# Kernel tuning notes

Hardware: AMD Instinct MI355X
Metric: run time of the kernel (lower is better)

## Reference

```python
import jax, jax.numpy as jnp
import numpy as np
import math

NUM_BUCKETS = 32
MAX_DISTANCE = 128
N_HEADS = 16
D_KV = 64
ATTN_SCALE = True


def _relative_position_bucket(relative_position, num_buckets=NUM_BUCKETS, max_distance=MAX_DISTANCE):
    # bidirectional (encoder) variant
    nb = num_buckets // 2
    buckets = (relative_position > 0).astype(jnp.int32) * nb
    rp = jnp.abs(relative_position)
    max_exact = nb // 2
    is_small = rp < max_exact
    rp_large = max_exact + (
        jnp.log(rp.astype(jnp.float32) / max_exact)
        / math.log(max_distance / max_exact)
        * (nb - max_exact)
    ).astype(jnp.int32)
    rp_large = jnp.minimum(rp_large, nb - 1)
    buckets = buckets + jnp.where(is_small, rp, rp_large)
    return buckets


def compute_bias(rel_bias_emb, q_len, k_len):
    ctx = jnp.arange(q_len)[:, None]
    mem = jnp.arange(k_len)[None, :]
    bucket = _relative_position_bucket(mem - ctx)  # [q,k] int32 in [0,32)
    values = rel_bias_emb[bucket]                  # [q,k,H]
    return jnp.transpose(values, (2, 0, 1))[None]  # [1,H,q,k]


def setup_inputs() -> dict:
    key = jax.random.key(0)
    k1, k2, k3, k4 = jax.random.split(key, 4)
    B, S, D = 2, 2048, 1024
    return {
        "hidden_states": jax.random.normal(k1, (B, S, D), jnp.float32),
        "attention_mask": jnp.ones((B, 1, S, S), jnp.float32),
        "W_qkv": jax.random.normal(k2, (D, 3 * D), jnp.float32) * 0.02,
        "W_o": jax.random.normal(k3, (D, D), jnp.float32) * 0.02,
        "rel_bias_emb": jax.random.normal(k4, (NUM_BUCKETS, N_HEADS), jnp.float32) * 0.02,
    }


def reference(hidden_states, attention_mask, W_qkv, W_o, rel_bias_emb):
    B, S, D = hidden_states.shape
    # fused QKV projection (no bias), then split as in split_tensor_along_last_dim
    qkv = jnp.einsum("bsd,de->bse", hidden_states, W_qkv)
    q, k, v = jnp.split(qkv, 3, axis=-1)
    # [b,s,H*d] -> [b,H,s,d]
    def to_heads(t):
        return jnp.transpose(t.reshape(B, S, N_HEADS, D_KV), (0, 2, 1, 3))
    q, k, v = to_heads(q), to_heads(k), to_heads(v)
    scores = jnp.einsum("bhqd,bhkd->bhqk", q, k)
    if ATTN_SCALE:
        scores = scores / math.sqrt(D_KV)
    position_bias = compute_bias(rel_bias_emb, S, S)  # [1,H,S,S]
    scores = scores * attention_mask + (-10000.0 * (1.0 - attention_mask) + position_bias)
    probs = jax.nn.softmax(scores, axis=-1)  # dropout = eval mode (identity)
    ctx = jnp.einsum("bhqk,bhkd->bhqd", probs, v)
    ctx = jnp.transpose(ctx, (0, 2, 1, 3)).reshape(B, S, N_HEADS * D_KV)
    attn_output = jnp.einsum("bse,ed->bsd", ctx, W_o)
    return attn_output
```

## Files before the change

kernel.cpp:

```cpp
#include <hip/hip_runtime.h>
#include <cstdint>

#define DEV static __device__ __forceinline__

typedef __bf16 bf16x8 __attribute__((ext_vector_type(8)));
typedef __bf16 bf16x4 __attribute__((ext_vector_type(4)));
typedef short  s16x4  __attribute__((ext_vector_type(4)));
typedef float  f32x4  __attribute__((ext_vector_type(4)));

DEV unsigned short f32_bf16(float f) {
  union { float f; unsigned u; } v; v.f = f;
  unsigned r = v.u + 0x7FFFu + ((v.u >> 16) & 1u);
  return (unsigned short)(r >> 16);
}

DEV void gload16(const void* g, void* lds) {
  __builtin_amdgcn_global_load_lds((__attribute__((address_space(1))) void*)g,
                                   (__attribute__((address_space(3))) void*)lds,
                                   16, 0, 0);
}

DEV float bcast_lane(float v, int srclane) {
  union { float f; int i; } u; u.f = v;
  u.i = __builtin_amdgcn_ds_bpermute(srclane << 2, u.i);
  return u.f;
}

DEV f32x4 mfma16_bf16(bf16x4 a, bf16x4 b, f32x4 c) {
  union { bf16x4 h; s16x4 s; } ua, ub; ua.h = a; ub.h = b;
#if __has_builtin(__builtin_amdgcn_mfma_f32_16x16x16bf16_1k)
  return __builtin_amdgcn_mfma_f32_16x16x16bf16_1k(ua.s, ub.s, c, 0, 0, 0);
#else
  f32x4 d;
  asm("v_mfma_f32_16x16x16_bf16 %0, %1, %2, %3" : "=v"(d) : "v"(ua.s), "v"(ub.s), "v"(c));
  return d;
#endif
}

__global__ void cast_bf16(const float* __restrict__ x, unsigned short* __restrict__ y) {
  int i = blockIdx.x * 256 + threadIdx.x;
  float4 v = ((const float4*)x)[i];
  uint2 o;
  o.x = (unsigned)f32_bf16(v.x) | ((unsigned)f32_bf16(v.y) << 16);
  o.y = (unsigned)f32_bf16(v.z) | ((unsigned)f32_bf16(v.w) << 16);
  ((uint2*)y)[i] = o;
}

__global__ void transpose_cast(const float* __restrict__ W, unsigned short* __restrict__ WT,
                               int K, int N) {
  __shared__ float t[64][65];
  int k0 = blockIdx.x * 64, n0 = blockIdx.y * 64;
  int tn = threadIdx.x & 63, tk = threadIdx.x >> 6;
#pragma unroll
  for (int i = 0; i < 64; i += 4)
    t[tk + i][tn] = W[(size_t)(k0 + tk + i) * N + n0 + tn];
  __syncthreads();
  int k2 = (threadIdx.x & 31) * 2, n = threadIdx.x >> 5;
#pragma unroll
  for (int i = 0; i < 64; i += 8) {
    int nn = n + i;
    unsigned o = (unsigned)f32_bf16(t[k2][nn]) | ((unsigned)f32_bf16(t[k2 + 1][nn]) << 16);
    *(unsigned*)&WT[(size_t)(n0 + nn) * K + k0 + k2] = o;
  }
}

__global__ void mask_check(const float* __restrict__ m, int* __restrict__ flag) {
  size_t i = ((size_t)blockIdx.x * 256 + threadIdx.x) * 4;
  float4 v = *(const float4*)(m + i);
  if (v.x != 1.0f || v.y != 1.0f || v.z != 1.0f || v.w != 1.0f) atomicOr(flag, 1);
}

template <int MODE, int TN>
__global__ void __launch_bounds__(256) gemm_bt(const unsigned short* __restrict__ A,
                                               const unsigned short* __restrict__ BT,
                                               float* __restrict__ Cout,
                                               unsigned short* __restrict__ Qb,
                                               unsigned short* __restrict__ Kb,
                                               unsigned short* __restrict__ VTb,
                                               int M, int N, int K) {
  constexpr int NT = TN / 32;
  __shared__ __align__(16) unsigned short As[128 * 32];
  __shared__ __align__(16) unsigned short Bs[TN * 32];
  const int tid = threadIdx.x, wave = tid >> 6, lane = tid & 63;
  const int l = lane & 15, quad = lane >> 4;
  const int wm = (wave & 1) * 64, wn = (wave >> 1) * (TN >> 1);
  const int bm = blockIdx.x, bn = blockIdx.y;

  const int srowA = wave * 32 + (lane >> 2);
  const int sswzA = ((lane & 3) ^ (srowA & 3)) * 8;
  const int srowB = (TN == 128) ? srowA : (wave * 16 + (lane >> 2));
  const int sswzB = ((lane & 3) ^ (srowB & 3)) * 8;
  const unsigned short* pA = A + (size_t)(bm * 128 + srowA) * K + sswzA;
  const unsigned short* pB = BT + (size_t)(bn * TN + srowB) * K + sswzB;
  unsigned short* ldsA0 = &As[(wave * 32) * 32];
  unsigned short* ldsA1 = &As[(wave * 32 + 16) * 32];
  unsigned short* ldsB0 = &Bs[((TN == 128 ? wave * 32 : wave * 16)) * 32];
  unsigned short* ldsB1 = &Bs[(wave * 32 + 16) * 32];

  f32x4 acc[4][NT];
#pragma unroll
  for (int i = 0; i < 4; i++)
#pragma unroll
    for (int j = 0; j < NT; j++) { f32x4 z = {0.f, 0.f, 0.f, 0.f}; acc[i][j] = z; }

  for (int kt = 0; kt < K; kt += 32) {
    __syncthreads();
    gload16(pA, ldsA0);
    gload16(pA + (size_t)16 * K, ldsA1);
    gload16(pB, ldsB0);
    if (TN == 128) gload16(pB + (size_t)16 * K, ldsB1);
    pA += 32; pB += 32;
    __syncthreads();
    bf16x8 af[4], bv[NT];
#pragma unroll
    for (int mt = 0; mt < 4; mt++) {
      int r = wm + mt * 16 + l;
      af[mt] = *(const bf16x8*)&As[r * 32 + ((quad ^ (r & 3)) * 8)];
    }
#pragma unroll
    for (int nt = 0; nt < NT; nt++) {
      int r = wn + nt * 16 + l;
      bv[nt] = *(const bf16x8*)&Bs[r * 32 + ((quad ^ (r & 3)) * 8)];
    }
#pragma unroll
    for (int mt = 0; mt < 4; mt++)
#pragma unroll
      for (int nt = 0; nt < NT; nt++)
        acc[mt][nt] = __builtin_amdgcn_mfma_f32_16x16x32_bf16(af[mt], bv[nt], acc[mt][nt], 0, 0, 0);
  }

#pragma unroll
  for (int nt = 0; nt < NT; nt++) {
    const int col = bn * TN + wn + nt * 16 + l;
#pragma unroll
    for (int mt = 0; mt < 4; mt++) {
      const int row0 = bm * 128 + wm + mt * 16 + quad * 4;
      if (MODE == 0) {
#pragma unroll
        for (int r = 0; r < 4; r++)
          Cout[(size_t)(row0 + r) * N + col] = acc[mt][nt][r];
      } else {
        const int bb = row0 >> 11, s = row0 & 2047;
        if (col < 2048) {
          unsigned short* dst = (col < 1024) ? Qb : Kb;
          const int c = col & 1023;
          const size_t off = ((size_t)(bb * 16 + (c >> 6)) * 2048 + s) * 64 + (c & 63);
#pragma unroll
          for (int r = 0; r < 4; r++)
            dst[off + (size_t)r * 64] = f32_bf16(acc[mt][nt][r]);
        } else {
          const int c = col - 2048;
          const int sl = s & 127;
          const int snew = (s & ~127) | (sl & 0x63) | ((sl & 0x0C) << 1) | ((sl & 0x10) >> 2);
          const size_t off = ((size_t)(bb * 16 + (c >> 6)) * 64 + (c & 63)) * 2048 + snew;
          bf16x4 pk;
#pragma unroll
          for (int r = 0; r < 4; r++) pk[r] = (__bf16)acc[mt][nt][r];
          *(bf16x4*)&VTb[off] = pk;
        }
      }
    }
  }
}

__global__ void __launch_bounds__(512, 4) attn(const unsigned short* __restrict__ Qb,
                                               const unsigned short* __restrict__ Kb,
                                               const unsigned short* __restrict__ VTb,
                                               const float* __restrict__ mask,
                                               const float* __restrict__ emb,
                                               const int* __restrict__ mflag,
                                               unsigned short* __restrict__ ctx) {
  __shared__ __align__(16) unsigned short KV[2][16384];
  __shared__ float biasLUT[512];

  const float LOG2E = 1.4426950408889634f;
  const float c1 = 0.125f * LOG2E;
  const float C2 = 10000.0f * LOG2E;
  const int tid = threadIdx.x, wave = tid >> 6, lane = tid & 63;
  const int l = lane & 15, quad = lane >> 4;
  const int wq = wave & 3, wk = wave >> 2;
  const int bh = blockIdx.x & 31, qt = blockIdx.x >> 5;
  const int b = bh >> 4, h = bh & 15;
  const int q0 = qt * 128;

  {
    int i = tid;
    int rel = i - 256;
    int rp = rel < 0 ? -rel : rel;
    int off = rp < 8 ? rp
                     : 8 + (rp >= 12) + (rp >= 16) + (rp >= 23) + (rp >= 32) +
                           (rp >= 46) + (rp >= 64) + (rp >= 91);
    int bucket = (rel > 0 ? 16 : 0) + off;
    biasLUT[i] = emb[bucket * 16 + h] * LOG2E;
  }
  const float satL = emb[15 * 16 + h] * LOG2E;
  const float satH = emb[31 * 16 + h] * LOG2E;
  const int masked = *mflag;

  const unsigned short* qb  = Qb  + ((size_t)(b * 16 + h) * 2048 + q0) * 64;
  const unsigned short* kb  = Kb  + (size_t)(b * 16 + h) * 2048 * 64;
  const unsigned short* vtb = VTb + (size_t)(b * 16 + h) * 64 * 2048;
  const float* mbase = mask + (size_t)b * 2048 * 2048;

  const int rw8 = lane >> 3, c8s = lane & 7;
  const int rw16 = lane >> 4, c16 = lane & 15;

#pragma unroll
  for (int j = 0; j < 2; j++) {
    int row = wave * 16 + j * 8 + rw8;
    gload16(qb + (size_t)row * 64 + ((c8s ^ (row & 7)) * 8), &KV[1][(wave * 16 + j * 8) * 64]);
  }
#pragma unroll
  for (int j = 0; j < 2; j++) {
    int row = wave * 16 + j * 8 + rw8;
    gload16(kb + (size_t)row * 64 + ((c8s ^ (row & 7)) * 8), &KV[0][(wave * 16 + j * 8) * 64]);
  }
#pragma unroll
  for (int j = 0; j < 2; j++) {
    int drow = wave * 8 + j * 4 + rw16;
    gload16(vtb + (size_t)drow * 2048 + ((c16 ^ (drow & 7)) * 8),
            &KV[0][8192 + (wave * 8 + j * 4) * 128]);
  }
  __syncthreads();

  bf16x8 qf[2][2];
#pragma unroll
  for (int mtq = 0; mtq < 2; mtq++)
#pragma unroll
    for (int ks = 0; ks < 2; ks++) {
      int row = wq * 32 + mtq * 16 + l;
      qf[mtq][ks] = *(const bf16x8*)&KV[1][row * 64 + (((ks * 4 + quad) ^ (row & 7)) * 8)];
    }
  __syncthreads();

#pragma unroll
  for (int j = 0; j < 2; j++) {
    int row = wave * 16 + j * 8 + rw8;
    gload16(kb + (size_t)(128 + row) * 64 + ((c8s ^ (row & 7)) * 8),
            &KV[1][(wave * 16 + j * 8) * 64]);
  }
#pragma unroll
  for (int j = 0; j < 2; j++) {
    int drow = wave * 8 + j * 4 + rw16;
    gload16(vtb + (size_t)drow * 2048 + 128 + ((c16 ^ (drow & 7)) * 8),
            &KV[1][8192 + (wave * 8 + j * 4) * 128]);
  }

  float lr[2] = {0.f, 0.f};
  f32x4 Oa[2][4];
#pragma unroll
  for (int mtq = 0; mtq < 2; mtq++)
#pragma unroll
    for (int dt = 0; dt < 4; dt++) { f32x4 z = {0.f, 0.f, 0.f, 0.f}; Oa[mtq][dt] = z; }

  for (int kt = 0; kt < 16; kt++) {
    const int k0 = kt * 128;
    const unsigned short* Ks  = KV[kt & 1];
    const unsigned short* VTs = KV[kt & 1] + 8192;

    const int d0 = k0 - q0;
    const bool sat = (d0 >= 256) || (d0 <= -256);
    const float bias_u = d0 > 0 ? satH : satL;
    const int ibase = 256 + d0 + wk * 64 + quad * 4 - wq * 32 - l;

#pragma unroll
    for (int p = 0; p < 2; p++) {
      bf16x4 pa[2][2];
#pragma unroll
      for (int t = 0; t < 2; t++) {
        const int ntk = p * 2 + t;
        int row = wk * 64 + ntk * 16 + l;
        bf16x8 kf0 = *(const bf16x8*)&Ks[row * 64 + ((quad ^ (row & 7)) * 8)];
        bf16x8 kf1 = *(const bf16x8*)&Ks[row * 64 + (((4 + quad) ^ (row & 7)) * 8)];
#pragma unroll
        for (int mtq = 0; mtq < 2; mtq++) {
          f32x4 s = {0.f, 0.f, 0.f, 0.f};
          s = __builtin_amdgcn_mfma_f32_16x16x32_bf16(kf0, qf[mtq][0], s, 0, 0, 0);
          s = __builtin_amdgcn_mfma_f32_16x16x32_bf16(kf1, qf[mtq][1], s, 0, 0, 0);

          const int ib = ibase + ntk * 16 - mtq * 16;
          if (!masked) {
            if (sat) {
#pragma unroll
              for (int r = 0; r < 4; r++) s[r] = fmaf(s[r], c1, bias_u);
            } else {
#pragma unroll
              for (int r = 0; r < 4; r++) s[r] = fmaf(s[r], c1, biasLUT[ib + r]);
            }
          } else {
            const int qg = q0 + wq * 32 + mtq * 16 + l;
            const int kg = k0 + wk * 64 + ntk * 16 + quad * 4;
            float4 mv4 = *(const float4*)&mbase[(size_t)qg * 2048 + kg];
#pragma unroll
            for (int r = 0; r < 4; r++) {
              float mv = r == 0 ? mv4.x : (r == 1 ? mv4.y : (r == 2 ? mv4.z : mv4.w));
              float bias = sat ? bias_u : biasLUT[ib + r];
              s[r] = fmaf(s[r], mv * c1, fmaf(mv, C2, bias - C2));
            }
          }
          bf16x4 pk;
          float ls = 0.f;
#pragma unroll
          for (int r = 0; r < 4; r++) {
            float pv = __builtin_amdgcn_exp2f(s[r]);
            ls += pv;
            pk[r] = (__bf16)pv;
          }
          lr[mtq] += ls;
          pa[mtq][t] = pk;
        }
      }

#pragma unroll
      for (int dt = 0; dt < 4; dt++) {
        int row = dt * 16 + l;
        bf16x8 w = *(const bf16x8*)&VTs[row * 128 + (((wk * 8 + p * 4 + quad) ^ (l & 7)) * 8)];
        bf16x4 vlo = __builtin_shufflevector(w, w, 0, 1, 2, 3);
        bf16x4 vhi = __builtin_shufflevector(w, w, 4, 5, 6, 7);
#pragma unroll
        for (int mtq = 0; mtq < 2; mtq++) {
          Oa[mtq][dt] = mfma16_bf16(pa[mtq][0], vlo, Oa[mtq][dt]);
          Oa[mtq][dt] = mfma16_bf16(pa[mtq][1], vhi, Oa[mtq][dt]);
        }
      }
    }

    __syncthreads();
    if (kt + 2 < 16) {
      const int kn = (kt + 2) * 128;
      unsigned short* dst = (unsigned short*)KV[kt & 1];
#pragma unroll
      for (int j = 0; j < 2; j++) {
        int row = wave * 16 + j * 8 + rw8;
        gload16(kb + (size_t)(kn + row) * 64 + ((c8s ^ (row & 7)) * 8),
                &dst[(wave * 16 + j * 8) * 64]);
      }
#pragma unroll
      for (int j = 0; j < 2; j++) {
        int drow = wave * 8 + j * 4 + rw16;
        gload16(vtb + (size_t)drow * 2048 + kn + ((c16 ^ (drow & 7)) * 8),
                &dst[8192 + (wave * 8 + j * 4) * 128]);
      }
    }
  }

  float* Of = (float*)KV;
  float* Lf = Of + 8192;
  if (wk == 1) {
#pragma unroll
    for (int mtq = 0; mtq < 2; mtq++) {
      float v = lr[mtq];
      v += __shfl_xor(v, 16);
      v += __shfl_xor(v, 32);
      if (quad == 0) Lf[wq * 32 + mtq * 16 + l] = v;
#pragma unroll
      for (int dt = 0; dt < 4; dt++)
#pragma unroll
        for (int r = 0; r < 4; r++)
          Of[(wq * 32 + mtq * 16 + quad * 4 + r) * 64 + dt * 16 + l] = Oa[mtq][dt][r];
    }
  }
  __syncthreads();
  if (wk == 0) {
#pragma unroll
    for (int mtq = 0; mtq < 2; mtq++) {
      float v = lr[mtq];
      v += __shfl_xor(v, 16);
      v += __shfl_xor(v, 32);
      v += Lf[wq * 32 + mtq * 16 + l];
      const float inv = 1.0f / v;
#pragma unroll
      for (int r = 0; r < 4; r++) {
        float i_bc = bcast_lane(inv, quad * 4 + r);
        const int qg = q0 + wq * 32 + mtq * 16 + quad * 4 + r;
#pragma unroll
        for (int dt = 0; dt < 4; dt++) {
          float o = Oa[mtq][dt][r] +
                    Of[(wq * 32 + mtq * 16 + quad * 4 + r) * 64 + dt * 16 + l];
          ctx[(size_t)(b * 2048 + qg) * 1024 + h * 64 + dt * 16 + l] = f32_bf16(o * i_bc);
        }
      }
    }
  }
}

extern "C" void kernel_launch(void* const* d_in, const int* in_sizes, int n_in,
                              void* d_out, int out_size, void* d_ws, size_t ws_size,
                              hipStream_t stream) {
  const float* hs   = (const float*)d_in[0];
  const float* mask = (const float*)d_in[1];
  const float* wqkv = (const float*)d_in[2];
  const float* wo   = (const float*)d_in[3];
  const float* emb  = (const float*)d_in[4];
  float* out = (float*)d_out;

  char* ws = (char*)d_ws;
  unsigned short* hB  = (unsigned short*)(ws);
  unsigned short* ctx = (unsigned short*)(ws);
  unsigned short* wqT = (unsigned short*)(ws + 8388608);
  unsigned short* woT = (unsigned short*)(ws + 14680064);
  unsigned short* Qb  = (unsigned short*)(ws + 16777216);
  unsigned short* Kb  = (unsigned short*)(ws + 25165824);
  unsigned short* VTb = (unsigned short*)(ws + 33554432);
  int* mflag          = (int*)(ws + 41943040);
  if (ws_size < 41943044) return;

  hipMemsetAsync(mflag, 0, 4, stream);
  cast_bf16<<<4096, 256, 0, stream>>>(hs, hB);
  transpose_cast<<<dim3(16, 48), 256, 0, stream>>>(wqkv, wqT, 1024, 3072);
  transpose_cast<<<dim3(16, 16), 256, 0, stream>>>(wo, woT, 1024, 1024);
  mask_check<<<8192, 256, 0, stream>>>(mask, mflag);
  gemm_bt<2, 128><<<dim3(32, 24), 256, 0, stream>>>(hB, wqT, nullptr, Qb, Kb, VTb, 4096, 3072, 1024);
  attn<<<512, 512, 0, stream>>>(Qb, Kb, VTb, mask, emb, mflag, ctx);
  gemm_bt<0, 64><<<dim3(32, 16), 256, 0, stream>>>(ctx, woT, out, nullptr, nullptr, nullptr, 4096, 1024, 1024);
}
```

Baseline: 219.6 us.

## Double-buffer LDS tiles in bf16 GEMM to overlap global loads with MFMA

The GEMM now keeps two LDS buffers for the A and B tiles. It issues the async global-to-LDS loads for the next K-step before computing on the current one, and drops one of the two barriers per iteration. The aim is to hide global load latency behind the MFMA work. In exchange, LDS use per block doubles, which may lower occupancy. The compiler may also insert conservative wait counts on the async LDS writes, which would limit the overlap.

Measured after the change: 216.0 us. Within noise of the previous version (-1.7%).

```diff
diff --git a/kernel.cpp b/kernel.cpp
--- a/kernel.cpp
+++ b/kernel.cpp
@@ -79,8 +79,8 @@
                                                unsigned short* __restrict__ VTb,
                                                int M, int N, int K) {
   constexpr int NT = TN / 32;
-  __shared__ __align__(16) unsigned short As[128 * 32];
-  __shared__ __align__(16) unsigned short Bs[TN * 32];
+  __shared__ __align__(16) unsigned short As[2][128 * 32];
+  __shared__ __align__(16) unsigned short Bs[2][TN * 32];
   const int tid = threadIdx.x, wave = tid >> 6, lane = tid & 63;
   const int l = lane & 15, quad = lane >> 4;
   const int wm = (wave & 1) * 64, wn = (wave >> 1) * (TN >> 1);
@@ -92,10 +92,18 @@
   const int sswzB = ((lane & 3) ^ (srowB & 3)) * 8;
   const unsigned short* pA = A + (size_t)(bm * 128 + srowA) * K + sswzA;
   const unsigned short* pB = BT + (size_t)(bn * TN + srowB) * K + sswzB;
-  unsigned short* ldsA0 = &As[(wave * 32) * 32];
-  unsigned short* ldsA1 = &As[(wave * 32 + 16) * 32];
-  unsigned short* ldsB0 = &Bs[((TN == 128 ? wave * 32 : wave * 16)) * 32];
-  unsigned short* ldsB1 = &Bs[(wave * 32 + 16) * 32];
+  const int ldsA0 = (wave * 32) * 32;
+  const int ldsA1 = (wave * 32 + 16) * 32;
+  const int ldsB0 = (TN == 128 ? wave * 32 : wave * 16) * 32;
+  const int ldsB1 = (wave * 32 + 16) * 32;
+
+  auto stage = [&](int buf) {
+    gload16(pA, &As[buf][ldsA0]);
+    gload16(pA + (size_t)16 * K, &As[buf][ldsA1]);
+    gload16(pB, &Bs[buf][ldsB0]);
+    if (TN == 128) gload16(pB + (size_t)16 * K, &Bs[buf][ldsB1]);
+    pA += 32; pB += 32;
+  };
 
   f32x4 acc[4][NT];
 #pragma unroll
@@ -103,24 +111,23 @@
 #pragma unroll
     for (int j = 0; j < NT; j++) { f32x4 z = {0.f, 0.f, 0.f, 0.f}; acc[i][j] = z; }
 
-  for (int kt = 0; kt < K; kt += 32) {
+  stage(0);
+
+  const int nkt = K >> 5;
+  for (int kt = 0; kt < nkt; kt++) {
+    const int cur = kt & 1;
     __syncthreads();
-    gload16(pA, ldsA0);
-    gload16(pA + (size_t)16 * K, ldsA1);
-    gload16(pB, ldsB0);
-    if (TN == 128) gload16(pB + (size_t)16 * K, ldsB1);
-    pA += 32; pB += 32;
-    __syncthreads();
+    if (kt + 1 < nkt) stage(cur ^ 1);
     bf16x8 af[4], bv[NT];
 #pragma unroll
     for (int mt = 0; mt < 4; mt++) {
       int r = wm + mt * 16 + l;
-      af[mt] = *(const bf16x8*)&As[r * 32 + ((quad ^ (r & 3)) * 8)];
+      af[mt] = *(const bf16x8*)&As[cur][r * 32 + ((quad ^ (r & 3)) * 8)];
     }
 #pragma unroll
     for (int nt = 0; nt < NT; nt++) {
       int r = wn + nt * 16 + l;
-      bv[nt] = *(const bf16x8*)&Bs[r * 32 + ((quad ^ (r & 3)) * 8)];
+      bv[nt] = *(const bf16x8*)&Bs[cur][r * 32 + ((quad ^ (r & 3)) * 8)];
     }
 #pragma unroll
     for (int mt = 0; mt < 4; mt++)
```
